# Optimization experiments

Hardware: AMD Instinct MI355X
Metric: run time of the kernel (lower is better)

## Reference

```python
import jax, jax.numpy as jnp
import numpy as np

B = 1048576          # batch of parallel trials; feature dims (12, 24) are fixed by the architecture
THRESH = 0.5         # braincog IFNode default threshold; mem starts at 0 so spike = (input > thresh)


def if_spike(i):
    # Fresh IFNode: mem = 0 + i ; spike = Heaviside(mem - threshold); mem reset where spiked (state unused here)
    return (i > THRESH).astype(i.dtype)


def setup_inputs() -> dict:
    key = jax.random.key(0)
    k1, k2 = jax.random.split(key)
    x1 = jax.random.uniform(k1, (B, 12), dtype=jnp.float32)
    x2 = jax.random.uniform(k2, (B, 24), dtype=jnp.float32)
    # Connection weights exactly as constructed in BNESNN.__init__
    W0 = jnp.eye(12, dtype=jnp.float32) * 6.0            # connection[0]
    W1 = jnp.zeros((12, 24), dtype=jnp.float32)          # connection[1]
    W2 = jnp.eye(24, dtype=jnp.float32) * 6.0            # connection[2]
    return {"x1": x1, "x2": x2, "W0": W0, "W1": W1, "W2": W2}


def reference(x1, x2, W0, W1, W2):
    # --- stdp[0] = STDP(node0, connection0) ---
    # i0 = CustomLinear: x1 @ W0 ; spikes via IF node; trace (fresh, decay irrelevant on 1st step) = x1
    i0 = x1 @ W0                      # [B, 12]
    s0 = if_spike(i0)                 # [B, 12] spikes (out__s)
    # dw0 = trace^T @ s0 is computed in torch but NOT returned by BNESNN.forward, so we skip it

    # --- stdp[1] = MutliInputSTDP(node1, [connection1, connection2]) ---
    i1 = s0 @ W1 + x2 @ W2            # [B, 24] summed synaptic currents
    s1 = if_spike(i1)                 # [B, 24] spikes (out__p)
    # autograd.grad(i1, [W1, W2], grad_outputs=s1) with inputs replaced in-place by their traces
    # (fresh traces == the inputs themselves): dw = trace^T @ s1
    dw1 = jnp.einsum('bi,bj->ij', s0, s1)   # [12, 24] grad wrt connection[1].weight
    dw2 = jnp.einsum('bi,bj->ij', x2, s1)   # [24, 24] grad wrt connection[2].weight

    # BNESNN.forward returns (dw, out__s, out__p) with dw = (dw1, dw2); flattened here
    return (dw1, dw2, s0, s1)
```

## Files before the change

### kernel.cpp

```cpp
#include <hip/hip_runtime.h>


typedef __bf16 bf16x8 __attribute__((ext_vector_type(8)));
typedef float  f32x4  __attribute__((ext_vector_type(4)));

constexpr int TPB  = 256;
constexpr int LDSS = 72;

__global__ void zero_dw_kernel(float* out) {
    int t = threadIdx.x + blockIdx.x * blockDim.x;
    if (t < 864) out[t] = 0.0f;
}

__device__ __forceinline__ void gload16(const float* g, float* lds) {
    __builtin_amdgcn_global_load_lds(
        (const __attribute__((address_space(1))) void*)(const void*)g,
        (__attribute__((address_space(3))) void*)(void*)lds, 16, 0, 0);
}

__global__ __launch_bounds__(TPB, 1)
void bnesnn_kernel(const float* __restrict__ x1, const float* __restrict__ x2,
                   const float* __restrict__ W0, const float* __restrict__ W1,
                   const float* __restrict__ W2, float* __restrict__ out, int B)
{
    __shared__ __attribute__((aligned(16))) float  xsh[4][3][2304];
    __shared__ __attribute__((aligned(16))) __bf16 aTs[4][36 * LDSS];
    __shared__ __attribute__((aligned(16))) __bf16 bTs[4][24 * LDSS];
    __shared__ __attribute__((aligned(16))) __bf16 zrow[LDSS];

    const int tid = threadIdx.x;
    const int w   = tid >> 6;
    const int l   = tid & 63;
    __bf16* aTw = aTs[w];
    __bf16* bTw = bTs[w];

    for (int i = tid; i < LDSS; i += TPB) zrow[i] = (__bf16)0.0f;

    bool okv = true;
    for (int i = tid; i < 144; i += TPB) if ((i / 12) != (i % 12) && W0[i] != 0.0f) okv = false;
    for (int i = tid; i < 288; i += TPB) if (W1[i] != 0.0f) okv = false;
    for (int i = tid; i < 576; i += TPB) if ((i / 24) != (i % 24) && W2[i] != 0.0f) okv = false;
    const int wdiag = __syncthreads_and(okv ? 1 : 0);
    const int fast  = wdiag && ((B & 255) == 0);

    float* s0out = out + 864;
    float* s1out = out + 864 + (size_t)12 * B;

    const int lrow = l & 15;
    const int kb   = (l >> 4) * 8;

    f32x4 acc[6] = {};

    const int NT = (B + 255) / 256;
    const int grid = gridDim.x;
    const int qn = NT / grid, rn = NT % grid;
    const int bid = blockIdx.x;
    const int t0  = (bid < rn) ? bid * (qn + 1) : rn * (qn + 1) + (bid - rn) * qn;
    const int t1  = t0 + ((bid < rn) ? qn + 1 : qn);
    const int n   = t1 - t0;

    auto mfmaPhase = [&]() {
        #pragma unroll
        for (int p = 0; p < 6; ++p) {
            const int arow = (p % 3) * 16 + lrow;
            const int brow = (p / 3) * 16 + lrow;
            const __bf16* ap = (arow < 36) ? (aTw + arow * LDSS + kb) : (zrow + kb);
            const __bf16* bp = (brow < 24) ? (bTw + brow * LDSS + kb) : (zrow + kb);
            #pragma unroll
            for (int kk = 0; kk < 64; kk += 32) {
                bf16x8 af = *(const bf16x8*)(ap + kk);
                bf16x8 bf = *(const bf16x8*)(bp + kk);
                acc[p] = __builtin_amdgcn_mfma_f32_16x16x32_bf16(af, bf, acc[p], 0, 0, 0);
            }
        }
    };

    if (fast) {
        f32x4 D0[3], D2[6];
        #pragma unroll
        for (int c = 0; c < 3; ++c) {
            D0[c][0] = W0[(4*c+0)*13]; D0[c][1] = W0[(4*c+1)*13];
            D0[c][2] = W0[(4*c+2)*13]; D0[c][3] = W0[(4*c+3)*13];
        }
        #pragma unroll
        for (int c = 0; c < 6; ++c) {
            D2[c][0] = W2[(4*c+0)*25]; D2[c][1] = W2[(4*c+1)*25];
            D2[c][2] = W2[(4*c+2)*25]; D2[c][3] = W2[(4*c+3)*25];
        }
        const int t3 = l % 3, t6 = l % 6;
        f32x4 e0[3], e2[6];
        #pragma unroll
        for (int k = 0; k < 3; ++k) {
            int i = (t3 + k) % 3;
            e0[k] = (i == 0) ? D0[0] : ((i == 1) ? D0[1] : D0[2]);
        }
        #pragma unroll
        for (int k = 0; k < 6; ++k) {
            int i = (t6 + 4 * k) % 6;
            e2[k] = (i == 0) ? D2[0] : ((i == 1) ? D2[1] : ((i == 2) ? D2[2] :
                    ((i == 3) ? D2[3] : ((i == 4) ? D2[4] : D2[5]))));
        }

        float4* q0 = (float4*)s0out;
        float4* q1 = (float4*)s1out;

        auto issueTile = [&](int tt, int dd) {
            const size_t b1 = (size_t)tt * 768  + (size_t)w * 192;
            const size_t b2 = (size_t)tt * 1536 + (size_t)w * 384;
            float* dst = &xsh[w][dd][0];
            const float* g1 = x1 + (b1 + (size_t)l) * 4;
            const float* g2 = x2 + (b2 + (size_t)l) * 4;
            #pragma unroll
            for (int k = 0; k < 3; ++k) gload16(g1 + k * 256, dst + k * 256);
            #pragma unroll
            for (int k = 0; k < 6; ++k) gload16(g2 + k * 256, dst + 768 + k * 256);
        };

        if (n >= 1) issueTile(t0, 0);
        if (n >= 2) issueTile(t0 + 1, 1);
        for (int i = 0; i < n; ++i) {
            const int t = t0 + i;
            if (i + 2 < n) issueTile(t + 2, (i + 2) % 3);
            {
                int la = n - 1 - i; if (la > 2) la = 2;
                int sa = i;         if (sa > 2) sa = 2;
                int cnt = 9 * (la + sa);
                if      (cnt == 0)  { asm volatile("s_waitcnt vmcnt(0)"  ::: "memory"); }
                else if (cnt == 9)  { asm volatile("s_waitcnt vmcnt(9)"  ::: "memory"); }
                else if (cnt == 18) { asm volatile("s_waitcnt vmcnt(18)" ::: "memory"); }
                else if (cnt == 27) { asm volatile("s_waitcnt vmcnt(27)" ::: "memory"); }
                else                { asm volatile("s_waitcnt vmcnt(36)" ::: "memory"); }
            }
            __builtin_amdgcn_sched_barrier(0);

            const float* xb = &xsh[w][i % 3][0];
            float4 buf[9];
            #pragma unroll
            for (int k = 0; k < 9; ++k) buf[k] = *(const float4*)&xb[k * 256 + l * 4];

            const size_t b1 = (size_t)t * 768  + (size_t)w * 192;
            const size_t b2 = (size_t)t * 1536 + (size_t)w * 384;

            #pragma unroll
            for (int k = 0; k < 3; ++k) {
                int q = k * 64 + l;
                int r = q / 3;
                int c = 4 * (q - 3 * r);
                float4 v = buf[k];
                f32x4  e = e0[k];
                float sa = (v.x * e[0] > 0.5f) ? 1.f : 0.f;
                float sb = (v.y * e[1] > 0.5f) ? 1.f : 0.f;
                float sc = (v.z * e[2] > 0.5f) ? 1.f : 0.f;
                float sd = (v.w * e[3] > 0.5f) ? 1.f : 0.f;
                q0[b1 + q] = make_float4(sa, sb, sc, sd);
                aTw[(c + 0) * LDSS + r] = (__bf16)sa;
                aTw[(c + 1) * LDSS + r] = (__bf16)sb;
                aTw[(c + 2) * LDSS + r] = (__bf16)sc;
                aTw[(c + 3) * LDSS + r] = (__bf16)sd;
            }
            #pragma unroll
            for (int k = 0; k < 6; ++k) {
                int q = k * 64 + l;
                int r = q / 6;
                int c = 4 * (q - 6 * r);
                float4 v = buf[3 + k];
                f32x4  e = e2[k];
                float sa = (v.x * e[0] > 0.5f) ? 1.f : 0.f;
                float sb = (v.y * e[1] > 0.5f) ? 1.f : 0.f;
                float sc = (v.z * e[2] > 0.5f) ? 1.f : 0.f;
                float sd = (v.w * e[3] > 0.5f) ? 1.f : 0.f;
                q1[b2 + q] = make_float4(sa, sb, sc, sd);
                aTw[(12 + c + 0) * LDSS + r] = (__bf16)v.x;
                aTw[(12 + c + 1) * LDSS + r] = (__bf16)v.y;
                aTw[(12 + c + 2) * LDSS + r] = (__bf16)v.z;
                aTw[(12 + c + 3) * LDSS + r] = (__bf16)v.w;
                bTw[(c + 0) * LDSS + r] = (__bf16)sa;
                bTw[(c + 1) * LDSS + r] = (__bf16)sb;
                bTw[(c + 2) * LDSS + r] = (__bf16)sc;
                bTw[(c + 3) * LDSS + r] = (__bf16)sd;
            }
            mfmaPhase();
        }
    } else {
        for (int t = t0; t < t1; ++t) {
            long r = (long)t * 256 + w * 64 + l;
            bool v = r < B;
            float xv[36];
            const float4 z = make_float4(0.f, 0.f, 0.f, 0.f);
            const float4* p1 = (const float4*)(x1 + r * 12);
            const float4* p2 = (const float4*)(x2 + r * 24);
            #pragma unroll
            for (int c = 0; c < 3; ++c) {
                float4 t4 = v ? p1[c] : z;
                xv[4*c+0] = t4.x; xv[4*c+1] = t4.y; xv[4*c+2] = t4.z; xv[4*c+3] = t4.w;
            }
            #pragma unroll
            for (int c = 0; c < 6; ++c) {
                float4 t4 = v ? p2[c] : z;
                xv[12+4*c+0] = t4.x; xv[12+4*c+1] = t4.y; xv[12+4*c+2] = t4.z; xv[12+4*c+3] = t4.w;
            }
            float s0v[12], s1v[24];
            #pragma unroll 1
            for (int j = 0; j < 12; ++j) {
                float a = 0.0f;
                for (int k = 0; k < 12; ++k) a += xv[k] * W0[k * 12 + j];
                s0v[j] = (a > 0.5f) ? 1.0f : 0.0f;
            }
            #pragma unroll 1
            for (int j = 0; j < 24; ++j) {
                float a = 0.0f;
                for (int k = 0; k < 12; ++k) a += s0v[k] * W1[k * 24 + j];
                for (int k = 0; k < 24; ++k) a += xv[12 + k] * W2[k * 24 + j];
                s1v[j] = (a > 0.5f) ? 1.0f : 0.0f;
            }
            if (v) {
                float4* q0 = (float4*)(s0out + (size_t)r * 12);
                q0[0] = make_float4(s0v[0], s0v[1], s0v[2],  s0v[3]);
                q0[1] = make_float4(s0v[4], s0v[5], s0v[6],  s0v[7]);
                q0[2] = make_float4(s0v[8], s0v[9], s0v[10], s0v[11]);
                float4* q1 = (float4*)(s1out + (size_t)r * 24);
                #pragma unroll
                for (int c = 0; c < 6; ++c)
                    q1[c] = make_float4(s1v[4*c+0], s1v[4*c+1], s1v[4*c+2], s1v[4*c+3]);
            }
            #pragma unroll
            for (int m = 0; m < 12; ++m) aTw[m * LDSS + l]        = (__bf16)(v ? s0v[m] : 0.f);
            #pragma unroll
            for (int m = 0; m < 24; ++m) aTw[(12 + m) * LDSS + l] = (__bf16)(v ? xv[12 + m] : 0.f);
            #pragma unroll
            for (int n2 = 0; n2 < 24; ++n2) bTw[n2 * LDSS + l]    = (__bf16)(v ? s1v[n2] : 0.f);
            mfmaPhase();
        }
    }

    __syncthreads();
    float* red = &xsh[0][0][0];
    #pragma unroll
    for (int p = 0; p < 6; ++p)
        *(f32x4*)&red[(w * 6 + p) * 256 + l * 4] = acc[p];
    __syncthreads();
    for (int e = tid; e < 1536; e += TPB) {
        int p  = e >> 8, le = e & 255;
        float s = red[p * 256 + le] + red[(6 + p) * 256 + le]
                + red[(12 + p) * 256 + le] + red[(18 + p) * 256 + le];
        int lane = le >> 2, i = le & 3;
        int m = (p % 3) * 16 + (lane >> 4) * 4 + i;
        int nn = (p / 3) * 16 + (lane & 15);
        if (m < 36 && nn < 24) {
            int addr = (m < 12) ? (m * 24 + nn) : (288 + (m - 12) * 24 + nn);
            atomicAdd(out + addr, s);
        }
    }
}

extern "C" void kernel_launch(void* const* d_in, const int* in_sizes, int n_in,
                              void* d_out, int out_size, void* d_ws, size_t ws_size,
                              hipStream_t stream) {
    const float* x1 = (const float*)d_in[0];
    const float* x2 = (const float*)d_in[1];
    const float* W0 = (const float*)d_in[2];
    const float* W1 = (const float*)d_in[3];
    const float* W2 = (const float*)d_in[4];
    float* out = (float*)d_out;
    const int B = in_sizes[0] / 12;
    if (B <= 0) return;

    zero_dw_kernel<<<dim3(4), dim3(256), 0, stream>>>(out);
    bnesnn_kernel<<<dim3(256), dim3(TPB), 0, stream>>>(x1, x2, W0, W1, W2, out, B);
}
```

Baseline: 68.76 us.

## Shrink blocks to two waves, pack LDS, and launch more blocks

Halves the block to 128 threads and replaces the per-wave LDS arrays with one packed 48KB buffer, so several blocks can share a CU. The grid grows from 256 to 768 blocks. The prefetch changes from a triple-buffered tile to a double-buffered x2 plus a single x1 buffer, whose next load is issued right after the current one is read. This trades prefetch depth for more resident waves, and relies on exact manual vmcnt accounting. The zero row is dropped, so padded MFMA rows now read neighbouring LDS regions.

```diff
diff --git a/kernel.cpp b/kernel.cpp
--- a/kernel.cpp
+++ b/kernel.cpp
@@ -4,7 +4,7 @@
 typedef __bf16 bf16x8 __attribute__((ext_vector_type(8)));
 typedef float  f32x4  __attribute__((ext_vector_type(4)));
 
-constexpr int TPB  = 256;
+constexpr int TPB  = 128;
 constexpr int LDSS = 72;
 
 __global__ void zero_dw_kernel(float* out) {
@@ -18,30 +18,27 @@
         (__attribute__((address_space(3))) void*)(void*)lds, 16, 0, 0);
 }
 
-__global__ __launch_bounds__(TPB, 1)
+__global__ __launch_bounds__(TPB, 2)
 void bnesnn_kernel(const float* __restrict__ x1, const float* __restrict__ x2,
                    const float* __restrict__ W0, const float* __restrict__ W1,
                    const float* __restrict__ W2, float* __restrict__ out, int B)
 {
-    __shared__ __attribute__((aligned(16))) float  xsh[4][3][2304];
-    __shared__ __attribute__((aligned(16))) __bf16 aTs[4][36 * LDSS];
-    __shared__ __attribute__((aligned(16))) __bf16 bTs[4][24 * LDSS];
-    __shared__ __attribute__((aligned(16))) __bf16 zrow[LDSS];
+    __shared__ __attribute__((aligned(16))) float smem[12000];
 
     const int tid = threadIdx.x;
     const int w   = tid >> 6;
     const int l   = tid & 63;
-    __bf16* aTw = aTs[w];
-    __bf16* bTw = bTs[w];
-
-    for (int i = tid; i < LDSS; i += TPB) zrow[i] = (__bf16)0.0f;
+    __bf16* bTw = (__bf16*)((char*)smem + (size_t)w * 3456);
+    __bf16* aTw = (__bf16*)((char*)smem + 6912 + (size_t)w * 5184);
+    float*  x2w = (float*)((char*)smem + 17280 + (size_t)w * 12288);
+    float*  x1w = (float*)((char*)smem + 41856 + (size_t)w * 3072);
 
     bool okv = true;
     for (int i = tid; i < 144; i += TPB) if ((i / 12) != (i % 12) && W0[i] != 0.0f) okv = false;
     for (int i = tid; i < 288; i += TPB) if (W1[i] != 0.0f) okv = false;
     for (int i = tid; i < 576; i += TPB) if ((i / 24) != (i % 24) && W2[i] != 0.0f) okv = false;
     const int wdiag = __syncthreads_and(okv ? 1 : 0);
-    const int fast  = wdiag && ((B & 255) == 0);
+    const int fast  = wdiag && ((B & 127) == 0);
 
     float* s0out = out + 864;
     float* s1out = out + 864 + (size_t)12 * B;
@@ -51,7 +48,7 @@
 
     f32x4 acc[6] = {};
 
-    const int NT = (B + 255) / 256;
+    const int NT = (B + 127) / 128;
     const int grid = gridDim.x;
     const int qn = NT / grid, rn = NT % grid;
     const int bid = blockIdx.x;
@@ -64,8 +61,8 @@
         for (int p = 0; p < 6; ++p) {
             const int arow = (p % 3) * 16 + lrow;
             const int brow = (p / 3) * 16 + lrow;
-            const __bf16* ap = (arow < 36) ? (aTw + arow * LDSS + kb) : (zrow + kb);
-            const __bf16* bp = (brow < 24) ? (bTw + brow * LDSS + kb) : (zrow + kb);
+            const __bf16* ap = aTw + arow * LDSS + kb;
+            const __bf16* bp = bTw + brow * LDSS + kb;
             #pragma unroll
             for (int kk = 0; kk < 64; kk += 32) {
                 bf16x8 af = *(const bf16x8*)(ap + kk);
@@ -104,42 +101,45 @@
         float4* q0 = (float4*)s0out;
         float4* q1 = (float4*)s1out;
 
-        auto issueTile = [&](int tt, int dd) {
-            const size_t b1 = (size_t)tt * 768  + (size_t)w * 192;
-            const size_t b2 = (size_t)tt * 1536 + (size_t)w * 384;
-            float* dst = &xsh[w][dd][0];
+        auto issueX2 = [&](int tt, int dd) {
+            const size_t b2 = (size_t)tt * 768 + (size_t)w * 384;
+            float* dst = x2w + dd * 1536;
+            const float* g2 = x2 + (b2 + (size_t)l) * 4;
+            #pragma unroll
+            for (int k = 0; k < 6; ++k) gload16(g2 + k * 256, dst + k * 256);
+        };
+        auto issueX1 = [&](int tt) {
+            const size_t b1 = (size_t)tt * 384 + (size_t)w * 192;
             const float* g1 = x1 + (b1 + (size_t)l) * 4;
-            const float* g2 = x2 + (b2 + (size_t)l) * 4;
-            #pragma unroll
-            for (int k = 0; k < 3; ++k) gload16(g1 + k * 256, dst + k * 256);
-            #pragma unroll
-            for (int k = 0; k < 6; ++k) gload16(g2 + k * 256, dst + 768 + k * 256);
+            #pragma unroll
+            for (int k = 0; k < 3; ++k) gload16(g1 + k * 256, x1w + k * 256);
         };
 
-        if (n >= 1) issueTile(t0, 0);
-        if (n >= 2) issueTile(t0 + 1, 1);
+        if (n >= 1) { issueX2(t0, 0); issueX1(t0); }
         for (int i = 0; i < n; ++i) {
             const int t = t0 + i;
-            if (i + 2 < n) issueTile(t + 2, (i + 2) % 3);
+            if (i + 1 < n) issueX2(t + 1, (i + 1) & 1);
             {
-                int la = n - 1 - i; if (la > 2) la = 2;
-                int sa = i;         if (sa > 2) sa = 2;
-                int cnt = 9 * (la + sa);
+                int cnt = 9 * (i > 0 ? 1 : 0) + 6 * (i < n - 1 ? 1 : 0);
                 if      (cnt == 0)  { asm volatile("s_waitcnt vmcnt(0)"  ::: "memory"); }
+                else if (cnt == 6)  { asm volatile("s_waitcnt vmcnt(6)"  ::: "memory"); }
                 else if (cnt == 9)  { asm volatile("s_waitcnt vmcnt(9)"  ::: "memory"); }
-                else if (cnt == 18) { asm volatile("s_waitcnt vmcnt(18)" ::: "memory"); }
-                else if (cnt == 27) { asm volatile("s_waitcnt vmcnt(27)" ::: "memory"); }
-                else                { asm volatile("s_waitcnt vmcnt(36)" ::: "memory"); }
+                else                { asm volatile("s_waitcnt vmcnt(15)" ::: "memory"); }
             }
             __builtin_amdgcn_sched_barrier(0);
 
-            const float* xb = &xsh[w][i % 3][0];
+            const float* xb2 = x2w + (i & 1) * 1536;
             float4 buf[9];
             #pragma unroll
-            for (int k = 0; k < 9; ++k) buf[k] = *(const float4*)&xb[k * 256 + l * 4];
-
-            const size_t b1 = (size_t)t * 768  + (size_t)w * 192;
-            const size_t b2 = (size_t)t * 1536 + (size_t)w * 384;
+            for (int k = 0; k < 3; ++k) buf[k]     = *(const float4*)&x1w[k * 256 + l * 4];
+            #pragma unroll
+            for (int k = 0; k < 6; ++k) buf[3 + k] = *(const float4*)&xb2[k * 256 + l * 4];
+            asm volatile("s_waitcnt lgkmcnt(0)" ::: "memory");
+            __builtin_amdgcn_sched_barrier(0);
+            if (i + 1 < n) issueX1(t + 1);
+
+            const size_t b1 = (size_t)t * 384 + (size_t)w * 192;
+            const size_t b2 = (size_t)t * 768 + (size_t)w * 384;
 
             #pragma unroll
             for (int k = 0; k < 3; ++k) {
@@ -183,7 +183,7 @@
         }
     } else {
         for (int t = t0; t < t1; ++t) {
-            long r = (long)t * 256 + w * 64 + l;
+            long r = (long)t * 128 + w * 64 + l;
             bool v = r < B;
             float xv[36];
             const float4 z = make_float4(0.f, 0.f, 0.f, 0.f);
@@ -234,15 +234,14 @@
     }
 
     __syncthreads();
-    float* red = &xsh[0][0][0];
+    float* red = smem;
     #pragma unroll
     for (int p = 0; p < 6; ++p)
         *(f32x4*)&red[(w * 6 + p) * 256 + l * 4] = acc[p];
     __syncthreads();
     for (int e = tid; e < 1536; e += TPB) {
         int p  = e >> 8, le = e & 255;
-        float s = red[p * 256 + le] + red[(6 + p) * 256 + le]
-                + red[(12 + p) * 256 + le] + red[(18 + p) * 256 + le];
+        float s = red[p * 256 + le] + red[(6 + p) * 256 + le];
         int lane = le >> 2, i = le & 3;
         int m = (p % 3) * 16 + (lane >> 4) * 4 + i;
         int nn = (p / 3) * 16 + (lane & 15);
@@ -266,5 +265,5 @@
     if (B <= 0) return;
 
     zero_dw_kernel<<<dim3(4), dim3(256), 0, stream>>>(out);
-    bnesnn_kernel<<<dim3(256), dim3(TPB), 0, stream>>>(x1, x2, W0, W1, W2, out, B);
-}
+    bnesnn_kernel<<<dim3(768), dim3(TPB), 0, stream>>>(x1, x2, W0, W1, W2, out, B);
+}
```

After: 90.66 us. 1.32x slower.

## Replace triple-buffered LDS prefetch with single buffer and higher occupancy

Applied to the files above, without the earlier changes.

Drops the per-wave three-stage global_load_lds prefetch pipeline. Each tile is now loaded into a single per-wave LDS region that also holds the bf16 transposed spike and trace tiles, with explicit waitcnts guarding the reuse. This cuts LDS per block enough to raise launch bounds to 4 blocks per CU and quadruple the grid, so latency is meant to be hidden by more resident waves instead of software prefetch. The zero-row padding is removed, so MFMA padding rows now read leftover LDS data that only feeds discarded output cells. Each wave also stalls on its own loads every iteration.

```diff
diff --git a/kernel.cpp b/kernel.cpp
--- a/kernel.cpp
+++ b/kernel.cpp
@@ -6,6 +6,7 @@
 
 constexpr int TPB  = 256;
 constexpr int LDSS = 72;
+constexpr int RWF  = 2448;
 
 __global__ void zero_dw_kernel(float* out) {
     int t = threadIdx.x + blockIdx.x * blockDim.x;
@@ -18,23 +19,19 @@
         (__attribute__((address_space(3))) void*)(void*)lds, 16, 0, 0);
 }
 
-__global__ __launch_bounds__(TPB, 1)
+__global__ __launch_bounds__(TPB, 4)
 void bnesnn_kernel(const float* __restrict__ x1, const float* __restrict__ x2,
                    const float* __restrict__ W0, const float* __restrict__ W1,
                    const float* __restrict__ W2, float* __restrict__ out, int B)
 {
-    __shared__ __attribute__((aligned(16))) float  xsh[4][3][2304];
-    __shared__ __attribute__((aligned(16))) __bf16 aTs[4][36 * LDSS];
-    __shared__ __attribute__((aligned(16))) __bf16 bTs[4][24 * LDSS];
-    __shared__ __attribute__((aligned(16))) __bf16 zrow[LDSS];
+    __shared__ __attribute__((aligned(16))) float smem[4 * RWF];
 
     const int tid = threadIdx.x;
     const int w   = tid >> 6;
     const int l   = tid & 63;
-    __bf16* aTw = aTs[w];
-    __bf16* bTw = bTs[w];
-
-    for (int i = tid; i < LDSS; i += TPB) zrow[i] = (__bf16)0.0f;
+    float*  xw  = smem + w * RWF;
+    __bf16* aTw = (__bf16*)xw;
+    __bf16* bTw = (__bf16*)(xw + 1296);
 
     bool okv = true;
     for (int i = tid; i < 144; i += TPB) if ((i / 12) != (i % 12) && W0[i] != 0.0f) okv = false;
@@ -57,15 +54,14 @@
     const int bid = blockIdx.x;
     const int t0  = (bid < rn) ? bid * (qn + 1) : rn * (qn + 1) + (bid - rn) * qn;
     const int t1  = t0 + ((bid < rn) ? qn + 1 : qn);
-    const int n   = t1 - t0;
 
     auto mfmaPhase = [&]() {
         #pragma unroll
         for (int p = 0; p < 6; ++p) {
             const int arow = (p % 3) * 16 + lrow;
             const int brow = (p / 3) * 16 + lrow;
-            const __bf16* ap = (arow < 36) ? (aTw + arow * LDSS + kb) : (zrow + kb);
-            const __bf16* bp = (brow < 24) ? (bTw + brow * LDSS + kb) : (zrow + kb);
+            const __bf16* ap = aTw + arow * LDSS + kb;
+            const __bf16* bp = bTw + brow * LDSS + kb;
             #pragma unroll
             for (int kk = 0; kk < 64; kk += 32) {
                 bf16x8 af = *(const bf16x8*)(ap + kk);
@@ -104,42 +100,28 @@
         float4* q0 = (float4*)s0out;
         float4* q1 = (float4*)s1out;
 
-        auto issueTile = [&](int tt, int dd) {
-            const size_t b1 = (size_t)tt * 768  + (size_t)w * 192;
-            const size_t b2 = (size_t)tt * 1536 + (size_t)w * 384;
-            float* dst = &xsh[w][dd][0];
-            const float* g1 = x1 + (b1 + (size_t)l) * 4;
-            const float* g2 = x2 + (b2 + (size_t)l) * 4;
-            #pragma unroll
-            for (int k = 0; k < 3; ++k) gload16(g1 + k * 256, dst + k * 256);
-            #pragma unroll
-            for (int k = 0; k < 6; ++k) gload16(g2 + k * 256, dst + 768 + k * 256);
-        };
-
-        if (n >= 1) issueTile(t0, 0);
-        if (n >= 2) issueTile(t0 + 1, 1);
-        for (int i = 0; i < n; ++i) {
-            const int t = t0 + i;
-            if (i + 2 < n) issueTile(t + 2, (i + 2) % 3);
-            {
-                int la = n - 1 - i; if (la > 2) la = 2;
-                int sa = i;         if (sa > 2) sa = 2;
-                int cnt = 9 * (la + sa);
-                if      (cnt == 0)  { asm volatile("s_waitcnt vmcnt(0)"  ::: "memory"); }
-                else if (cnt == 9)  { asm volatile("s_waitcnt vmcnt(9)"  ::: "memory"); }
-                else if (cnt == 18) { asm volatile("s_waitcnt vmcnt(18)" ::: "memory"); }
-                else if (cnt == 27) { asm volatile("s_waitcnt vmcnt(27)" ::: "memory"); }
-                else                { asm volatile("s_waitcnt vmcnt(36)" ::: "memory"); }
-            }
+        for (int t = t0; t < t1; ++t) {
+            asm volatile("s_waitcnt lgkmcnt(0)" ::: "memory");
             __builtin_amdgcn_sched_barrier(0);
-
-            const float* xb = &xsh[w][i % 3][0];
-            float4 buf[9];
-            #pragma unroll
-            for (int k = 0; k < 9; ++k) buf[k] = *(const float4*)&xb[k * 256 + l * 4];
 
             const size_t b1 = (size_t)t * 768  + (size_t)w * 192;
             const size_t b2 = (size_t)t * 1536 + (size_t)w * 384;
+            {
+                const float* g1 = x1 + (b1 + (size_t)l) * 4;
+                const float* g2 = x2 + (b2 + (size_t)l) * 4;
+                #pragma unroll
+                for (int k = 0; k < 3; ++k) gload16(g1 + k * 256, xw + k * 256);
+                #pragma unroll
+                for (int k = 0; k < 6; ++k) gload16(g2 + k * 256, xw + 768 + k * 256);
+            }
+            asm volatile("s_waitcnt vmcnt(0)" ::: "memory");
+            __builtin_amdgcn_sched_barrier(0);
+
+            float4 buf[9];
+            #pragma unroll
+            for (int k = 0; k < 9; ++k) buf[k] = *(const float4*)&xw[k * 256 + l * 4];
+            asm volatile("s_waitcnt lgkmcnt(0)" ::: "memory");
+            __builtin_amdgcn_sched_barrier(0);
 
             #pragma unroll
             for (int k = 0; k < 3; ++k) {
@@ -183,6 +165,7 @@
         }
     } else {
         for (int t = t0; t < t1; ++t) {
+            asm volatile("s_waitcnt lgkmcnt(0)" ::: "memory");
             long r = (long)t * 256 + w * 64 + l;
             bool v = r < B;
             float xv[36];
@@ -234,7 +217,7 @@
     }
 
     __syncthreads();
-    float* red = &xsh[0][0][0];
+    float* red = smem;
     #pragma unroll
     for (int p = 0; p < 6; ++p)
         *(f32x4*)&red[(w * 6 + p) * 256 + l * 4] = acc[p];
@@ -266,5 +249,5 @@
     if (B <= 0) return;
 
     zero_dw_kernel<<<dim3(4), dim3(256), 0, stream>>>(out);
-    bnesnn_kernel<<<dim3(256), dim3(TPB), 0, stream>>>(x1, x2, W0, W1, W2, out, B);
-}
+    bnesnn_kernel<<<dim3(1024), dim3(TPB), 0, stream>>>(x1, x2, W0, W1, W2, out, B);
+}
```

Measured after the change: 137.9 us. 2.01x slower.
